# Optimization experiments

Hardware: AMD Instinct MI355X
Metric: run time of the kernel (lower is better)

Reference implementation:

```python
import jax, jax.numpy as jnp
import numpy as np

B, S, D, H = 4, 2048, 1024, 16
HD = D // H


def setup_inputs() -> dict:
    key = jax.random.key(0)
    ks = jax.random.split(key, 12)
    sc = 0.02
    inp = {
        "q": jax.random.normal(ks[0], (B, S, D), jnp.float32),
        "k": jax.random.normal(ks[1], (B, S, D), jnp.float32),
        "v": jax.random.normal(ks[2], (B, S, D), jnp.float32),
        "mask": jnp.tril(jnp.ones((S, S), jnp.int32))[None, None],  # causal [1,1,S,S]
        "Wq": jax.random.normal(ks[3], (D, D), jnp.float32) * sc,
        "bq": jnp.zeros((D,), jnp.float32),
        "Wk": jax.random.normal(ks[4], (D, D), jnp.float32) * sc,
        "bk": jnp.zeros((D,), jnp.float32),
        "Wv": jax.random.normal(ks[5], (D, D), jnp.float32) * sc,
        "bv": jnp.zeros((D,), jnp.float32),
        "Wo": jax.random.normal(ks[6], (D, D), jnp.float32) * sc,
        "bo": jnp.zeros((D,), jnp.float32),
    }
    return inp


def reference(q, k, v, mask, Wq, bq, Wk, bk, Wv, bv, Wo, bo):
    # Linear projections (torch Linear: x @ W.T + b)
    qh = (q @ Wq.T + bq).reshape(B, S, H, HD).transpose(0, 2, 1, 3)  # [B,H,S,hd]
    kh = (k @ Wk.T + bk).reshape(B, S, H, HD).transpose(0, 2, 1, 3)
    vh = (v @ Wv.T + bv).reshape(B, S, H, HD).transpose(0, 2, 1, 3)
    score = jnp.einsum("bhqd,bhkd->bhqk", qh, kh) / jnp.sqrt(jnp.float32(HD))
    score = jnp.where(mask == 0, jnp.float32(-10000.0), score)
    attn = jax.nn.softmax(score, axis=-1)
    out = jnp.einsum("bhqk,bhkd->bhqd", attn, vh)  # [B,H,S,hd]
    out = out.transpose(0, 2, 1, 3).reshape(B, S, D)
    return out @ Wo.T + bo
```

## Files before the change

### kernel.cpp

```cpp
#include <hip/hip_runtime.h>

#define S_LEN 2048
#define D_DIM 1024
#define NB    4
#define NH    16
#define HDIM  64
#define PLD   72
#define QSCL  0.18033688011112042f

typedef float  f32x4  __attribute__((ext_vector_type(4)));
typedef __bf16 bf16x4 __attribute__((ext_vector_type(4)));
typedef __bf16 bf16x8 __attribute__((ext_vector_type(8)));

static __device__ __forceinline__ f32x4 mfma16(bf16x8 a, bf16x8 b, f32x4 c) {
  return __builtin_amdgcn_mfma_f32_16x16x32_bf16(a, b, c, 0, 0, 0);
}
static __device__ __forceinline__ bf16x4 cvt4(f32x4 v) {
  return __builtin_convertvector(v, bf16x4);
}
static __device__ __forceinline__ bf16x8 cvt8(f32x4 lo, f32x4 hi) {
  bf16x4 a = cvt4(lo), b = cvt4(hi);
  bf16x8 r;
  r[0] = a[0]; r[1] = a[1]; r[2] = a[2]; r[3] = a[3];
  r[4] = b[0]; r[5] = b[1]; r[6] = b[2]; r[7] = b[3];
  return r;
}
static __device__ __forceinline__ void cp16(const void* g, void* l) {
  __builtin_amdgcn_global_load_lds(
      (const __attribute__((address_space(1))) unsigned int*)g,
      (__attribute__((address_space(3))) unsigned int*)l, 16, 0, 0);
}

__global__ __launch_bounds__(256) void conv_w(
    const float* __restrict__ Wq, const float* __restrict__ Wk,
    const float* __restrict__ Wv, const float* __restrict__ Wo,
    __bf16* __restrict__ out)
{
  const float* src;
  if (blockIdx.y == 0) src = Wq;
  else if (blockIdx.y == 1) src = Wk;
  else if (blockIdx.y == 2) src = Wv;
  else src = Wo;
  size_t i = ((size_t)blockIdx.x * 256 + threadIdx.x) * 4;
  f32x4 v = *(const f32x4*)(src + i);
  *(bf16x4*)(out + (size_t)blockIdx.y * (D_DIM * D_DIM) + i) = cvt4(v);
}

__global__ __launch_bounds__(256) void conv_a(
    const float* __restrict__ q, const float* __restrict__ k,
    const float* __restrict__ v, __bf16* __restrict__ out)
{
  const float* src;
  if (blockIdx.y == 0) src = q;
  else if (blockIdx.y == 1) src = k;
  else src = v;
  size_t i = ((size_t)blockIdx.x * 256 + threadIdx.x) * 4;
  f32x4 x = *(const f32x4*)(src + i);
  *(bf16x4*)(out + (size_t)blockIdx.y * ((size_t)NB * S_LEN * D_DIM) + i) = cvt4(x);
}

static __device__ __forceinline__ void proj_epilogue(
    f32x4 (&acc)[4][4], int z, int mbase, int nbase, int wm, int wn,
    int l15, int quad, const float* bias,
    __bf16* qh, __bf16* kh, __bf16* vt)
{
  const float scl = (z == 0) ? QSCL : 1.0f;
#pragma unroll
  for (int mt = 0; mt < 4; ++mt)
#pragma unroll
    for (int nt = 0; nt < 4; ++nt) {
      int n = nbase + wn + nt * 16 + l15;
      int h = n >> 6, hd = n & 63;
      float bb = bias[n];
      f32x4 vv = acc[mt][nt];
#pragma unroll
      for (int r = 0; r < 4; ++r) vv[r] = (vv[r] + bb) * scl;
      bf16x4 pv = cvt4(vv);
      int m0 = mbase + wm + mt * 16 + quad * 4;
      int b = m0 >> 11, s0 = m0 & 2047;
      if (z == 2) {
        *(bf16x4*)(vt + ((size_t)((b * NH + h) * HDIM + hd)) * S_LEN + s0) = pv;
      } else {
        __bf16* out = (z == 0) ? qh : kh;
#pragma unroll
        for (int r = 0; r < 4; ++r)
          out[((size_t)(b * NH + h) * S_LEN + s0 + r) * HDIM + hd] = pv[r];
      }
    }
}

__global__ __launch_bounds__(256, 4) void proj_bf16(
    const __bf16* __restrict__ abf, const __bf16* __restrict__ Wbf,
    const float* __restrict__ bq, const float* __restrict__ bk, const float* __restrict__ bv,
    __bf16* __restrict__ qh, __bf16* __restrict__ kh, __bf16* __restrict__ vt)
{
  const __bf16* A = abf + (size_t)blockIdx.z * ((size_t)NB * S_LEN * D_DIM);
  const __bf16* W = Wbf + (size_t)blockIdx.z * (D_DIM * D_DIM);
  const float* bias = (blockIdx.z == 0) ? bq : (blockIdx.z == 1) ? bk : bv;

  __shared__ __bf16 As[128 * 64];
  __shared__ __bf16 Bs[128 * 64];

  const int tid  = threadIdx.x;
  const int wave = tid >> 6;
  const int lane = tid & 63;
  const int l15  = lane & 15;
  const int quad = lane >> 4;
  const int mbase = blockIdx.x * 128;
  const int nbase = blockIdx.y * 128;
  const int wm = (wave & 1) * 64;
  const int wn = (wave >> 1) * 64;
  const int brow = lane >> 3;
  const int scol = ((lane & 7) ^ (brow & 7)) * 8;
  const int swz  = l15 & 7;

  f32x4 acc[4][4] = {};

  for (int kt = 0; kt < D_DIM; kt += 64) {
#pragma unroll
    for (int c = 0; c < 4; ++c) {
      int r = wave * 32 + c * 8 + brow;
      cp16(A + (size_t)(mbase + r) * D_DIM + kt + scol, As + r * 64);
      cp16(W + (size_t)(nbase + r) * D_DIM + kt + scol, Bs + r * 64);
    }
    __syncthreads();

#pragma unroll
    for (int k0 = 0; k0 < 2; ++k0) {
      bf16x8 af[4], bfr[4];
#pragma unroll
      for (int i = 0; i < 4; ++i) {
        int off = ((k0 * 4 + quad) ^ swz) * 8;
        af[i]  = *(const bf16x8*)(As + (wm + i * 16 + l15) * 64 + off);
        bfr[i] = *(const bf16x8*)(Bs + (wn + i * 16 + l15) * 64 + off);
      }
#pragma unroll
      for (int mt = 0; mt < 4; ++mt)
#pragma unroll
        for (int nt = 0; nt < 4; ++nt)
          acc[mt][nt] = mfma16(af[mt], bfr[nt], acc[mt][nt]);
    }
    __syncthreads();
  }

  proj_epilogue(acc, blockIdx.z, mbase, nbase, wm, wn, l15, quad, bias, qh, kh, vt);
}

__global__ __launch_bounds__(256, 2) void proj_f32(
    const float* __restrict__ qin, const float* __restrict__ kin, const float* __restrict__ vin,
    const __bf16* __restrict__ Wbf,
    const float* __restrict__ bq, const float* __restrict__ bk, const float* __restrict__ bv,
    __bf16* __restrict__ qh, __bf16* __restrict__ kh, __bf16* __restrict__ vt)
{
  const float* A; const float* bias;
  if (blockIdx.z == 0)      { A = qin; bias = bq; }
  else if (blockIdx.z == 1) { A = kin; bias = bk; }
  else                      { A = vin; bias = bv; }
  const __bf16* W = Wbf + (size_t)blockIdx.z * (D_DIM * D_DIM);

  __shared__ float  As[128 * 64];
  __shared__ __bf16 Bs[128 * 64];

  const int tid  = threadIdx.x;
  const int wave = tid >> 6;
  const int lane = tid & 63;
  const int l15  = lane & 15;
  const int quad = lane >> 4;
  const int mbase = blockIdx.x * 128;
  const int nbase = blockIdx.y * 128;
  const int wm = (wave & 1) * 64;
  const int wn = (wave >> 1) * 64;
  const int arow = lane >> 4;
  const int brow = lane >> 3;

  f32x4 acc[4][4] = {};

  for (int kt = 0; kt < D_DIM; kt += 64) {
#pragma unroll
    for (int c = 0; c < 8; ++c) {
      int rr = c * 4 + arow;
      int r  = wave * 32 + rr;
      int col = ((lane & 15) ^ (rr & 15)) * 4;
      cp16(A + (size_t)(mbase + r) * D_DIM + kt + col, As + r * 64);
    }
#pragma unroll
    for (int c = 0; c < 4; ++c) {
      int r  = wave * 32 + c * 8 + brow;
      int col = ((lane & 7) ^ (brow & 7)) * 8;
      cp16(W + (size_t)(nbase + r) * D_DIM + kt + col, Bs + r * 64);
    }
    __syncthreads();

#pragma unroll
    for (int k0 = 0; k0 < 2; ++k0) {
      bf16x8 af[4], bfr[4];
#pragma unroll
      for (int i = 0; i < 4; ++i) {
        const float* ap = As + (wm + i * 16 + l15) * 64;
        int c0 = k0 * 8 + quad * 2;
        f32x4 lo = *(const f32x4*)(ap + ((c0 ^ l15) * 4));
        f32x4 hi = *(const f32x4*)(ap + (((c0 + 1) ^ l15) * 4));
        af[i] = cvt8(lo, hi);
        bfr[i] = *(const bf16x8*)(Bs + (wn + i * 16 + l15) * 64 +
                                  (((k0 * 4 + quad) ^ (l15 & 7)) * 8));
      }
#pragma unroll
      for (int mt = 0; mt < 4; ++mt)
#pragma unroll
        for (int nt = 0; nt < 4; ++nt)
          acc[mt][nt] = mfma16(af[mt], bfr[nt], acc[mt][nt]);
    }
    __syncthreads();
  }

  proj_epilogue(acc, blockIdx.z, mbase, nbase, wm, wn, l15, quad, bias, qh, kh, vt);
}

__global__ __launch_bounds__(256, 4) void attn_kernel(
    const __bf16* __restrict__ qh, const __bf16* __restrict__ kh,
    const __bf16* __restrict__ vt, __bf16* __restrict__ ao)
{
  __shared__ __bf16 Kb[64 * 64];
  __shared__ __bf16 Vb[64 * 64];
  __shared__ __bf16 Ps[4][2][16 * PLD];

  const int bh = blockIdx.y;
  const int x  = blockIdx.x;
  const int qc0 = x, qc1 = 31 - x;
  const __bf16* qp = qh + (size_t)bh * S_LEN * HDIM;
  const __bf16* kp = kh + (size_t)bh * S_LEN * HDIM;
  const __bf16* vp = vt + (size_t)bh * HDIM * S_LEN;

  const int tid  = threadIdx.x;
  const int wave = tid >> 6;
  const int lane = tid & 63;
  const int l15  = lane & 15;
  const int quad = lane >> 4;
  const int w16  = wave * 16;
  const int srow = lane >> 3;
  const int scol = ((lane & 7) ^ srow) * 8;
  const int swz  = l15 & 7;
  const int b = bh >> 4, h = bh & 15;

  bf16x8 fq[2][2];
#pragma unroll
  for (int j = 0; j < 2; ++j) {
    const int qb = (j ? qc1 : qc0) * 64;
    const __bf16* qrow = qp + (size_t)(qb + w16 + l15) * HDIM;
    fq[j][0] = *(const bf16x8*)(qrow + quad * 8);
    fq[j][1] = *(const bf16x8*)(qrow + 32 + quad * 8);
  }

  f32x4 accO[2][4] = {};
  float lp[2] = {0.f, 0.f};

  for (int kt = 0; kt <= qc1; ++kt) {
    __syncthreads();
#pragma unroll
    for (int c = 0; c < 2; ++c) {
      int rb = w16 + c * 8;
      cp16(kp + (size_t)(kt * 64 + rb + srow) * HDIM + scol,  &Kb[rb * 64]);
      cp16(vp + (size_t)(rb + srow) * S_LEN + kt * 64 + scol, &Vb[rb * 64]);
    }
    __syncthreads();

    const bool act0 = (kt <= qc0);

    f32x4 sc[2][4] = {};
#pragma unroll
    for (int k0 = 0; k0 < 2; ++k0)
#pragma unroll
      for (int nt = 0; nt < 4; ++nt) {
        bf16x8 bk = *(const bf16x8*)(Kb + (nt * 16 + l15) * 64 + (((k0 * 4 + quad) ^ swz) * 8));
        if (act0) sc[0][nt] = mfma16(bk, fq[0][k0], sc[0][nt]);
        sc[1][nt] = mfma16(bk, fq[1][k0], sc[1][nt]);
      }

#pragma unroll
    for (int j = 0; j < 2; ++j) {
      if (j == 0 && !act0) continue;
      const int qcj = j ? qc1 : qc0;
      __bf16* wp = &Ps[wave][j][0];
      float ls = 0.f;
      if (kt == qcj) {
#pragma unroll
        for (int nt = 0; nt < 4; ++nt) {
          f32x4 p;
#pragma unroll
          for (int r = 0; r < 4; ++r) {
            float pv = __builtin_amdgcn_exp2f(sc[j][nt][r]);
            if (nt * 16 + quad * 4 + r > w16 + l15) pv = 0.f;
            ls += pv;
            p[r] = pv;
          }
          *(bf16x4*)(wp + l15 * PLD + nt * 16 + quad * 4) = cvt4(p);
        }
      } else {
#pragma unroll
        for (int nt = 0; nt < 4; ++nt) {
          f32x4 p;
#pragma unroll
          for (int r = 0; r < 4; ++r) {
            float pv = __builtin_amdgcn_exp2f(sc[j][nt][r]);
            ls += pv;
            p[r] = pv;
          }
          *(bf16x4*)(wp + l15 * PLD + nt * 16 + quad * 4) = cvt4(p);
        }
      }
      lp[j] += ls;
    }

#pragma unroll
    for (int k0 = 0; k0 < 2; ++k0) {
      bf16x8 ap0, ap1;
      if (act0) ap0 = *(const bf16x8*)(&Ps[wave][0][0] + l15 * PLD + k0 * 32 + quad * 8);
      ap1 = *(const bf16x8*)(&Ps[wave][1][0] + l15 * PLD + k0 * 32 + quad * 8);
#pragma unroll
      for (int nt = 0; nt < 4; ++nt) {
        bf16x8 bv = *(const bf16x8*)(Vb + (nt * 16 + l15) * 64 + (((k0 * 4 + quad) ^ swz) * 8));
        if (act0) accO[0][nt] = mfma16(ap0, bv, accO[0][nt]);
        accO[1][nt] = mfma16(ap1, bv, accO[1][nt]);
      }
    }
  }

#pragma unroll
  for (int j = 0; j < 2; ++j) {
    float lf = lp[j];
    lf += __shfl_xor(lf, 16);
    lf += __shfl_xor(lf, 32);
    const int qb = (j ? qc1 : qc0) * 64;
#pragma unroll
    for (int r = 0; r < 4; ++r) {
      float inv = 1.0f / __shfl(lf, quad * 4 + r);
      f32x4 dummy;
      (void)dummy;
#pragma unroll
      for (int nt = 0; nt < 4; ++nt) {
      }
#pragma unroll
      for (int nt = 0; nt < 4; ++nt) accO[j][nt][r] *= inv;
    }
#pragma unroll
    for (int nt = 0; nt < 4; ++nt) {
      bf16x4 ob = cvt4(accO[j][nt]);
#pragma unroll
      for (int r = 0; r < 4; ++r) {
        int sr = qb + w16 + quad * 4 + r;
        ao[((size_t)b * S_LEN + sr) * D_DIM + h * HDIM + nt * 16 + l15] = ob[r];
      }
    }
  }
}

__global__ __launch_bounds__(256, 4) void out_gemm(
    const __bf16* __restrict__ Ain, const __bf16* __restrict__ Wbf,
    const float* __restrict__ bo, float* __restrict__ Cout)
{
  __shared__ __bf16 As[128 * 64];
  __shared__ __bf16 Bs[128 * 64];

  const int tid  = threadIdx.x;
  const int wave = tid >> 6;
  const int lane = tid & 63;
  const int l15  = lane & 15;
  const int quad = lane >> 4;
  const int mbase = blockIdx.x * 128;
  const int nbase = blockIdx.y * 128;
  const int wm = (wave & 1) * 64;
  const int wn = (wave >> 1) * 64;
  const int brow = lane >> 3;
  const int scol = ((lane & 7) ^ (brow & 7)) * 8;
  const int swz  = l15 & 7;

  f32x4 acc[4][4] = {};

  for (int kt = 0; kt < D_DIM; kt += 64) {
#pragma unroll
    for (int c = 0; c < 4; ++c) {
      int r = wave * 32 + c * 8 + brow;
      cp16(Ain + (size_t)(mbase + r) * D_DIM + kt + scol, As + r * 64);
      cp16(Wbf + (size_t)(nbase + r) * D_DIM + kt + scol, Bs + r * 64);
    }
    __syncthreads();

#pragma unroll
    for (int k0 = 0; k0 < 2; ++k0) {
      bf16x8 af[4], bfr[4];
#pragma unroll
      for (int i = 0; i < 4; ++i) {
        int off = ((k0 * 4 + quad) ^ swz) * 8;
        af[i]  = *(const bf16x8*)(As + (wm + i * 16 + l15) * 64 + off);
        bfr[i] = *(const bf16x8*)(Bs + (wn + i * 16 + l15) * 64 + off);
      }
#pragma unroll
      for (int mt = 0; mt < 4; ++mt)
#pragma unroll
        for (int nt = 0; nt < 4; ++nt)
          acc[mt][nt] = mfma16(af[mt], bfr[nt], acc[mt][nt]);
    }
    __syncthreads();
  }

#pragma unroll
  for (int mt = 0; mt < 4; ++mt)
#pragma unroll
    for (int nt = 0; nt < 4; ++nt) {
      int n = nbase + wn + nt * 16 + l15;
      float bb = bo[n];
      int m0 = mbase + wm + mt * 16 + quad * 4;
#pragma unroll
      for (int r = 0; r < 4; ++r)
        Cout[(size_t)(m0 + r) * D_DIM + n] = acc[mt][nt][r] + bb;
    }
}

extern "C" void kernel_launch(void* const* d_in, const int* in_sizes, int n_in,
                              void* d_out, int out_size, void* d_ws, size_t ws_size,
                              hipStream_t stream) {
  const float* q  = (const float*)d_in[0];
  const float* k  = (const float*)d_in[1];
  const float* v  = (const float*)d_in[2];
  const float* Wq = (const float*)d_in[4];
  const float* bq = (const float*)d_in[5];
  const float* Wk = (const float*)d_in[6];
  const float* bk = (const float*)d_in[7];
  const float* Wv = (const float*)d_in[8];
  const float* bv = (const float*)d_in[9];
  const float* Wo = (const float*)d_in[10];
  const float* bo = (const float*)d_in[11];

  __bf16* ws = (__bf16*)d_ws;
  const size_t WSZ = (size_t)D_DIM * D_DIM;
  const size_t NE  = (size_t)NB * S_LEN * D_DIM;
  __bf16* wbf = ws;
  __bf16* qh  = ws + 4 * WSZ;
  __bf16* kh  = qh + NE;
  __bf16* vt  = kh + NE;
  __bf16* ao  = vt + NE;
  __bf16* abf = vt + NE;
  const size_t NEED = (size_t)(4 * WSZ + 6 * NE) * sizeof(__bf16);

  const bool useBf16A = (ws_size >= NEED);

  conv_w<<<dim3(1024, 4), 256, 0, stream>>>(Wq, Wk, Wv, Wo, wbf);
  if (useBf16A) {
    conv_a<<<dim3(8192, 3), 256, 0, stream>>>(q, k, v, abf);
    proj_bf16<<<dim3(64, 8, 3), 256, 0, stream>>>(abf, wbf, bq, bk, bv, qh, kh, vt);
  } else {
    proj_f32<<<dim3(64, 8, 3), 256, 0, stream>>>(q, k, v, wbf, bq, bk, bv, qh, kh, vt);
  }
  attn_kernel<<<dim3(16, 64), 256, 0, stream>>>(qh, kh, vt, ao);
  out_gemm<<<dim3(64, 8), 256, 0, stream>>>(ao, wbf + 3 * WSZ, bo, (float*)d_out);
}
```

Measured before the change: 307.9 us.

## Process four query tiles per attention block with double-buffered K/V loads

Each attention workgroup now handles four causally balanced 64-row query tiles instead of two, so every K/V tile staged in LDS feeds twice as many MFMAs. K/V loads are double-buffered to prefetch the next tile during compute, and the P buffer drops its padded stride in favour of an XOR swizzle. Blocks are also remapped so that neighbouring block IDs fall in different heads. The grid halves to 512 blocks and launch bounds drop to 2 blocks per CU, which raises register and LDS use and lowers the number of waves available to hide latency.

```diff
diff --git a/kernel.cpp b/kernel.cpp
--- a/kernel.cpp
+++ b/kernel.cpp
@@ -5,7 +5,6 @@
 #define NB    4
 #define NH    16
 #define HDIM  64
-#define PLD   72
 #define QSCL  0.18033688011112042f
 
 typedef float  f32x4  __attribute__((ext_vector_type(4)));
@@ -216,17 +215,22 @@
   proj_epilogue(acc, blockIdx.z, mbase, nbase, wm, wn, l15, quad, bias, qh, kh, vt);
 }
 
-__global__ __launch_bounds__(256, 4) void attn_kernel(
+__global__ __launch_bounds__(256, 2) void attn_kernel(
     const __bf16* __restrict__ qh, const __bf16* __restrict__ kh,
     const __bf16* __restrict__ vt, __bf16* __restrict__ ao)
 {
-  __shared__ __bf16 Kb[64 * 64];
-  __shared__ __bf16 Vb[64 * 64];
-  __shared__ __bf16 Ps[4][2][16 * PLD];
-
-  const int bh = blockIdx.y;
-  const int x  = blockIdx.x;
-  const int qc0 = x, qc1 = 31 - x;
+  __shared__ __bf16 Kb[2][64 * 64];
+  __shared__ __bf16 Vb[2][64 * 64];
+  __shared__ __bf16 Ps[4][4][16 * 64];
+
+  const int lin = blockIdx.x + (blockIdx.y << 3);
+  const int my  = (lin & 7) * 64 + (lin >> 3);
+  const int x   = my & 7;
+  const int bh  = my >> 3;
+
+  const int qcs[4] = { x, 31 - x, x + 8, 23 - x };
+  const int last = 31 - x;
+
   const __bf16* qp = qh + (size_t)bh * S_LEN * HDIM;
   const __bf16* kp = kh + (size_t)bh * S_LEN * HDIM;
   const __bf16* vp = vt + (size_t)bh * HDIM * S_LEN;
@@ -242,47 +246,68 @@
   const int swz  = l15 & 7;
   const int b = bh >> 4, h = bh & 15;
 
-  bf16x8 fq[2][2];
-#pragma unroll
-  for (int j = 0; j < 2; ++j) {
-    const int qb = (j ? qc1 : qc0) * 64;
+  bf16x8 fq[4][2];
+#pragma unroll
+  for (int j = 0; j < 4; ++j) {
+    const int qb = qcs[j] * 64;
     const __bf16* qrow = qp + (size_t)(qb + w16 + l15) * HDIM;
     fq[j][0] = *(const bf16x8*)(qrow + quad * 8);
     fq[j][1] = *(const bf16x8*)(qrow + 32 + quad * 8);
   }
 
-  f32x4 accO[2][4] = {};
-  float lp[2] = {0.f, 0.f};
-
-  for (int kt = 0; kt <= qc1; ++kt) {
-    __syncthreads();
-#pragma unroll
-    for (int c = 0; c < 2; ++c) {
-      int rb = w16 + c * 8;
-      cp16(kp + (size_t)(kt * 64 + rb + srow) * HDIM + scol,  &Kb[rb * 64]);
-      cp16(vp + (size_t)(rb + srow) * S_LEN + kt * 64 + scol, &Vb[rb * 64]);
-    }
-    __syncthreads();
-
-    const bool act0 = (kt <= qc0);
-
-    f32x4 sc[2][4] = {};
+  f32x4 accO[4][4] = {};
+  float lp[4] = {0.f, 0.f, 0.f, 0.f};
+
+#pragma unroll
+  for (int c = 0; c < 2; ++c) {
+    int rb = w16 + c * 8;
+    cp16(kp + (size_t)(rb + srow) * HDIM + scol,  &Kb[0][rb * 64]);
+    cp16(vp + (size_t)(rb + srow) * S_LEN + scol, &Vb[0][rb * 64]);
+  }
+
+  int cur = 0;
+  for (int kt = 0; kt <= last; ++kt) {
+    __syncthreads();
+
+    if (kt < last) {
+#pragma unroll
+      for (int c = 0; c < 2; ++c) {
+        int rb = w16 + c * 8;
+        cp16(kp + (size_t)((kt + 1) * 64 + rb + srow) * HDIM + scol,
+             &Kb[cur ^ 1][rb * 64]);
+        cp16(vp + (size_t)(rb + srow) * S_LEN + (kt + 1) * 64 + scol,
+             &Vb[cur ^ 1][rb * 64]);
+      }
+    }
+
+    const __bf16* Kc = &Kb[cur][0];
+    const __bf16* Vc = &Vb[cur][0];
+
+    f32x4 sc[4][4];
+#pragma unroll
+    for (int j = 0; j < 4; ++j)
+      if (kt <= qcs[j])
+#pragma unroll
+        for (int nt = 0; nt < 4; ++nt) sc[j][nt] = (f32x4){0.f, 0.f, 0.f, 0.f};
+
 #pragma unroll
     for (int k0 = 0; k0 < 2; ++k0)
 #pragma unroll
       for (int nt = 0; nt < 4; ++nt) {
-        bf16x8 bk = *(const bf16x8*)(Kb + (nt * 16 + l15) * 64 + (((k0 * 4 + quad) ^ swz) * 8));
-        if (act0) sc[0][nt] = mfma16(bk, fq[0][k0], sc[0][nt]);
-        sc[1][nt] = mfma16(bk, fq[1][k0], sc[1][nt]);
-      }
-
-#pragma unroll
-    for (int j = 0; j < 2; ++j) {
-      if (j == 0 && !act0) continue;
-      const int qcj = j ? qc1 : qc0;
+        bf16x8 bk = *(const bf16x8*)(Kc + (nt * 16 + l15) * 64 +
+                                     (((k0 * 4 + quad) ^ swz) * 8));
+#pragma unroll
+        for (int j = 0; j < 4; ++j)
+          if (kt <= qcs[j]) sc[j][nt] = mfma16(bk, fq[j][k0], sc[j][nt]);
+      }
+
+#pragma unroll
+    for (int j = 0; j < 4; ++j) {
+      if (kt > qcs[j]) continue;
       __bf16* wp = &Ps[wave][j][0];
+      const int g0 = ((quad >> 1) ^ swz) * 8 + (quad & 1) * 4;
       float ls = 0.f;
-      if (kt == qcj) {
+      if (kt == qcs[j]) {
 #pragma unroll
         for (int nt = 0; nt < 4; ++nt) {
           f32x4 p;
@@ -293,7 +318,8 @@
             ls += pv;
             p[r] = pv;
           }
-          *(bf16x4*)(wp + l15 * PLD + nt * 16 + quad * 4) = cvt4(p);
+          *(bf16x4*)(wp + l15 * 64 +
+                     (((nt * 2 + (quad >> 1)) ^ swz) * 8) + (quad & 1) * 4) = cvt4(p);
         }
       } else {
 #pragma unroll
@@ -305,40 +331,44 @@
             ls += pv;
             p[r] = pv;
           }
-          *(bf16x4*)(wp + l15 * PLD + nt * 16 + quad * 4) = cvt4(p);
+          *(bf16x4*)(wp + l15 * 64 +
+                     (((nt * 2 + (quad >> 1)) ^ swz) * 8) + (quad & 1) * 4) = cvt4(p);
         }
       }
       lp[j] += ls;
+      (void)g0;
     }
 
 #pragma unroll
     for (int k0 = 0; k0 < 2; ++k0) {
-      bf16x8 ap0, ap1;
-      if (act0) ap0 = *(const bf16x8*)(&Ps[wave][0][0] + l15 * PLD + k0 * 32 + quad * 8);
-      ap1 = *(const bf16x8*)(&Ps[wave][1][0] + l15 * PLD + k0 * 32 + quad * 8);
+      bf16x8 ap[4];
+#pragma unroll
+      for (int j = 0; j < 4; ++j)
+        if (kt <= qcs[j])
+          ap[j] = *(const bf16x8*)(&Ps[wave][j][0] + l15 * 64 +
+                                   (((k0 * 4 + quad) ^ swz) * 8));
 #pragma unroll
       for (int nt = 0; nt < 4; ++nt) {
-        bf16x8 bv = *(const bf16x8*)(Vb + (nt * 16 + l15) * 64 + (((k0 * 4 + quad) ^ swz) * 8));
-        if (act0) accO[0][nt] = mfma16(ap0, bv, accO[0][nt]);
-        accO[1][nt] = mfma16(ap1, bv, accO[1][nt]);
-      }
-    }
-  }
-
-#pragma unroll
-  for (int j = 0; j < 2; ++j) {
+        bf16x8 bv = *(const bf16x8*)(Vc + (nt * 16 + l15) * 64 +
+                                     (((k0 * 4 + quad) ^ swz) * 8));
+#pragma unroll
+        for (int j = 0; j < 4; ++j)
+          if (kt <= qcs[j]) accO[j][nt] = mfma16(ap[j], bv, accO[j][nt]);
+      }
+    }
+
+    cur ^= 1;
+  }
+
+#pragma unroll
+  for (int j = 0; j < 4; ++j) {
     float lf = lp[j];
     lf += __shfl_xor(lf, 16);
     lf += __shfl_xor(lf, 32);
-    const int qb = (j ? qc1 : qc0) * 64;
+    const int qb = qcs[j] * 64;
 #pragma unroll
     for (int r = 0; r < 4; ++r) {
       float inv = 1.0f / __shfl(lf, quad * 4 + r);
-      f32x4 dummy;
-      (void)dummy;
-#pragma unroll
-      for (int nt = 0; nt < 4; ++nt) {
-      }
 #pragma unroll
       for (int nt = 0; nt < 4; ++nt) accO[j][nt][r] *= inv;
     }
@@ -451,6 +481,6 @@
   } else {
     proj_f32<<<dim3(64, 8, 3), 256, 0, stream>>>(q, k, v, wbf, bq, bk, bv, qh, kh, vt);
   }
-  attn_kernel<<<dim3(16, 64), 256, 0, stream>>>(qh, kh, vt, ao);
+  attn_kernel<<<dim3(8, 64), 256, 0, stream>>>(qh, kh, vt, ao);
   out_gemm<<<dim3(64, 8), 256, 0, stream>>>(ao, wbf + 3 * WSZ, bo, (float*)d_out);
 }
```

Measured after the change: 326.1 us. 1.06x slower.

## Double-buffer K/V tiles, shuffle P in registers, remap blocks across XCDs

Applied to the files above, without the earlier changes.

The attention kernel now prefetches the next K/V tile into a second LDS buffer while computing on the current one, which drops one barrier per iteration. It also replaces the P round-trip through shared memory with cross-lane shuffles that build the MFMA A-operand directly in registers. Blocks are remapped so that heads are grouped per XCD and causal workloads are interleaved for better L2 locality and balance. The extra shuffles add VALU work, and the doubled K/V buffers change the LDS footprint and possibly occupancy. The prefetch relies on the single barrier at the top of the next iteration to complete the async LDS loads.

```diff
diff --git a/kernel.cpp b/kernel.cpp
--- a/kernel.cpp
+++ b/kernel.cpp
@@ -5,12 +5,13 @@
 #define NB    4
 #define NH    16
 #define HDIM  64
-#define PLD   72
 #define QSCL  0.18033688011112042f
 
 typedef float  f32x4  __attribute__((ext_vector_type(4)));
 typedef __bf16 bf16x4 __attribute__((ext_vector_type(4)));
 typedef __bf16 bf16x8 __attribute__((ext_vector_type(8)));
+typedef unsigned int u32x2 __attribute__((ext_vector_type(2)));
+typedef unsigned int u32x4 __attribute__((ext_vector_type(4)));
 
 static __device__ __forceinline__ f32x4 mfma16(bf16x8 a, bf16x8 b, f32x4 c) {
   return __builtin_amdgcn_mfma_f32_16x16x32_bf16(a, b, c, 0, 0, 0);
@@ -220,13 +221,19 @@
     const __bf16* __restrict__ qh, const __bf16* __restrict__ kh,
     const __bf16* __restrict__ vt, __bf16* __restrict__ ao)
 {
-  __shared__ __bf16 Kb[64 * 64];
-  __shared__ __bf16 Vb[64 * 64];
-  __shared__ __bf16 Ps[4][2][16 * PLD];
-
-  const int bh = blockIdx.y;
-  const int x  = blockIdx.x;
+  __shared__ __bf16 Kb[2][64 * 64];
+  __shared__ __bf16 Vb[2][64 * 64];
+
+  const int lin = blockIdx.x + (blockIdx.y << 4);
+  const int xcd = lin & 7;
+  const int idx = lin >> 3;
+  const int u   = idx & 15;
+  const int x   = (u & 1) ? (15 - (u >> 1)) : (u >> 1);
+  const int bh  = xcd * 8 + (idx >> 4);
+
   const int qc0 = x, qc1 = 31 - x;
+  const int last = qc1;
+
   const __bf16* qp = qh + (size_t)bh * S_LEN * HDIM;
   const __bf16* kp = kh + (size_t)bh * S_LEN * HDIM;
   const __bf16* vp = vt + (size_t)bh * HDIM * S_LEN;
@@ -242,6 +249,10 @@
   const int swz  = l15 & 7;
   const int b = bh >> 4, h = bh & 15;
 
+  const int srcA = l15 + ((lane & 16) << 1);
+  const int srcB = srcA + 16;
+  const bool hiq = (lane & 32) != 0;
+
   bf16x8 fq[2][2];
 #pragma unroll
   for (int j = 0; j < 2; ++j) {
@@ -254,16 +265,30 @@
   f32x4 accO[2][4] = {};
   float lp[2] = {0.f, 0.f};
 
-  for (int kt = 0; kt <= qc1; ++kt) {
-    __syncthreads();
-#pragma unroll
-    for (int c = 0; c < 2; ++c) {
-      int rb = w16 + c * 8;
-      cp16(kp + (size_t)(kt * 64 + rb + srow) * HDIM + scol,  &Kb[rb * 64]);
-      cp16(vp + (size_t)(rb + srow) * S_LEN + kt * 64 + scol, &Vb[rb * 64]);
-    }
-    __syncthreads();
-
+#pragma unroll
+  for (int c = 0; c < 2; ++c) {
+    int rb = w16 + c * 8;
+    cp16(kp + (size_t)(rb + srow) * HDIM + scol,  &Kb[0][rb * 64]);
+    cp16(vp + (size_t)(rb + srow) * S_LEN + scol, &Vb[0][rb * 64]);
+  }
+
+  int cur = 0;
+  for (int kt = 0; kt <= last; ++kt) {
+    __syncthreads();
+
+    if (kt < last) {
+#pragma unroll
+      for (int c = 0; c < 2; ++c) {
+        int rb = w16 + c * 8;
+        cp16(kp + (size_t)((kt + 1) * 64 + rb + srow) * HDIM + scol,
+             &Kb[cur ^ 1][rb * 64]);
+        cp16(vp + (size_t)(rb + srow) * S_LEN + (kt + 1) * 64 + scol,
+             &Vb[cur ^ 1][rb * 64]);
+      }
+    }
+
+    const __bf16* Kc = &Kb[cur][0];
+    const __bf16* Vc = &Vb[cur][0];
     const bool act0 = (kt <= qc0);
 
     f32x4 sc[2][4] = {};
@@ -271,58 +296,62 @@
     for (int k0 = 0; k0 < 2; ++k0)
 #pragma unroll
       for (int nt = 0; nt < 4; ++nt) {
-        bf16x8 bk = *(const bf16x8*)(Kb + (nt * 16 + l15) * 64 + (((k0 * 4 + quad) ^ swz) * 8));
+        bf16x8 bk = *(const bf16x8*)(Kc + (nt * 16 + l15) * 64 +
+                                     (((k0 * 4 + quad) ^ swz) * 8));
         if (act0) sc[0][nt] = mfma16(bk, fq[0][k0], sc[0][nt]);
         sc[1][nt] = mfma16(bk, fq[1][k0], sc[1][nt]);
       }
 
+    bf16x8 pa[2][2];
 #pragma unroll
     for (int j = 0; j < 2; ++j) {
       if (j == 0 && !act0) continue;
       const int qcj = j ? qc1 : qc0;
-      __bf16* wp = &Ps[wave][j][0];
-      float ls = 0.f;
-      if (kt == qcj) {
-#pragma unroll
-        for (int nt = 0; nt < 4; ++nt) {
-          f32x4 p;
-#pragma unroll
-          for (int r = 0; r < 4; ++r) {
-            float pv = __builtin_amdgcn_exp2f(sc[j][nt][r]);
-            if (nt * 16 + quad * 4 + r > w16 + l15) pv = 0.f;
-            ls += pv;
-            p[r] = pv;
-          }
-          *(bf16x4*)(wp + l15 * PLD + nt * 16 + quad * 4) = cvt4(p);
+      unsigned int d0[4], d1[4];
+      float lsn[4];
+#pragma unroll
+      for (int nt = 0; nt < 4; ++nt) {
+        f32x4 p;
+#pragma unroll
+        for (int r = 0; r < 4; ++r) p[r] = __builtin_amdgcn_exp2f(sc[j][nt][r]);
+        if (kt == qcj) {
+#pragma unroll
+          for (int r = 0; r < 4; ++r)
+            if (nt * 16 + quad * 4 + r > w16 + l15) p[r] = 0.f;
         }
-      } else {
-#pragma unroll
-        for (int nt = 0; nt < 4; ++nt) {
-          f32x4 p;
-#pragma unroll
-          for (int r = 0; r < 4; ++r) {
-            float pv = __builtin_amdgcn_exp2f(sc[j][nt][r]);
-            ls += pv;
-            p[r] = pv;
-          }
-          *(bf16x4*)(wp + l15 * PLD + nt * 16 + quad * 4) = cvt4(p);
-        }
-      }
-      lp[j] += ls;
-    }
-
-#pragma unroll
-    for (int k0 = 0; k0 < 2; ++k0) {
-      bf16x8 ap0, ap1;
-      if (act0) ap0 = *(const bf16x8*)(&Ps[wave][0][0] + l15 * PLD + k0 * 32 + quad * 8);
-      ap1 = *(const bf16x8*)(&Ps[wave][1][0] + l15 * PLD + k0 * 32 + quad * 8);
+        lsn[nt] = (p[0] + p[1]) + (p[2] + p[3]);
+        u32x2 w = __builtin_bit_cast(u32x2, cvt4(p));
+        d0[nt] = w[0]; d1[nt] = w[1];
+      }
+      lp[j] += (lsn[0] + lsn[1]) + (lsn[2] + lsn[3]);
+
+      u32x4 A0, A1;
+#pragma unroll
+      for (int dw = 0; dw < 4; ++dw) {
+        const unsigned int* dd = (dw & 1) ? d1 : d0;
+        const int src = (dw < 2) ? srcA : srcB;
+        unsigned int t0 = (unsigned int)__shfl((int)dd[0], src);
+        unsigned int t1 = (unsigned int)__shfl((int)dd[1], src);
+        unsigned int t2 = (unsigned int)__shfl((int)dd[2], src);
+        unsigned int t3 = (unsigned int)__shfl((int)dd[3], src);
+        A0[dw] = hiq ? t1 : t0;
+        A1[dw] = hiq ? t3 : t2;
+      }
+      pa[j][0] = __builtin_bit_cast(bf16x8, A0);
+      pa[j][1] = __builtin_bit_cast(bf16x8, A1);
+    }
+
+#pragma unroll
+    for (int k0 = 0; k0 < 2; ++k0)
 #pragma unroll
       for (int nt = 0; nt < 4; ++nt) {
-        bf16x8 bv = *(const bf16x8*)(Vb + (nt * 16 + l15) * 64 + (((k0 * 4 + quad) ^ swz) * 8));
-        if (act0) accO[0][nt] = mfma16(ap0, bv, accO[0][nt]);
-        accO[1][nt] = mfma16(ap1, bv, accO[1][nt]);
-      }
-    }
+        bf16x8 bv = *(const bf16x8*)(Vc + (nt * 16 + l15) * 64 +
+                                     (((k0 * 4 + quad) ^ swz) * 8));
+        if (act0) accO[0][nt] = mfma16(pa[0][k0], bv, accO[0][nt]);
+        accO[1][nt] = mfma16(pa[1][k0], bv, accO[1][nt]);
+      }
+
+    cur ^= 1;
   }
 
 #pragma unroll
@@ -334,11 +363,6 @@
 #pragma unroll
     for (int r = 0; r < 4; ++r) {
       float inv = 1.0f / __shfl(lf, quad * 4 + r);
-      f32x4 dummy;
-      (void)dummy;
-#pragma unroll
-      for (int nt = 0; nt < 4; ++nt) {
-      }
 #pragma unroll
       for (int nt = 0; nt < 4; ++nt) accO[j][nt][r] *= inv;
     }
```

Result: slower. 332.5 us (+8.0%).
